# Optimization experiments

Hardware: AMD Instinct MI355X
Metric: run time of the kernel (lower is better)

Reference implementation:

```python
import jax, jax.numpy as jnp
import numpy as np

COMMITMENT_COST = 0.25


def setup_inputs() -> dict:
    key = jax.random.key(0)
    k1, k2 = jax.random.split(key)
    inputs = jax.random.normal(k1, (64, 4096, 64), dtype=jnp.float32)
    codewords = jax.random.normal(k2, (512, 64), dtype=jnp.float32)
    return {"inputs": inputs, "codewords": codewords}


def reference(inputs, codewords):
    D = codewords.shape[-1]
    flat = inputs.reshape(-1, D)  # (N, D)
    # squared Euclidean distances (N, K) via expansion, avoiding the (N, K, D) tensor
    x_sq = jnp.sum(flat * flat, axis=-1, keepdims=True)          # (N, 1)
    c_sq = jnp.sum(codewords * codewords, axis=-1)               # (K,)
    distances = x_sq - 2.0 * (flat @ codewords.T) + c_sq         # (N, K)
    encoding_indices = jnp.argmin(distances, axis=1)             # (N,)
    quantized = jnp.take(codewords, encoding_indices, axis=0).reshape(inputs.shape)
    commitment_loss = jnp.mean((jax.lax.stop_gradient(quantized) - inputs) ** 2)
    loss = COMMITMENT_COST * commitment_loss
    encoding_indices = encoding_indices.reshape(inputs.shape[:-1])
    return quantized, encoding_indices, loss
```

## Files before the change

kernel.cpp:

```cpp
#include <hip/hip_runtime.h>


typedef _Float16 half8 __attribute__((ext_vector_type(8)));
typedef float    floatx4 __attribute__((ext_vector_type(4)));

#define NVEC  262144
#define DDIM  64
#define KCW   512
#define LOSS_SCALE (0.25f / 16777216.0f)
#define DMARGIN 0.005f
#define BROWS 256
#define NBLK  (NVEC / BROWS)
#define CHUNK 256

#define SM_BS     0
#define SM_CSQH   69632
#define SM_WIN    71680
#define SM_LIST   72704
#define SM_FLG    73728
#define SM_RED    73984
#define SM_CNT    74016
#define SMEM_BYTES 74112

#define WS_CSQ   0
#define WS_CSQH  2048

__global__ void prep_kernel(const float* __restrict__ cw,
                            float* __restrict__ csq,
                            float* __restrict__ csqh,
                            float* __restrict__ loss_slot) {
    int n = blockIdx.x * blockDim.x + threadIdx.x;
    if (n < KCW) {
        const float4* r = (const float4*)(cw + n * DDIM);
        float s = 0.f;
        #pragma unroll
        for (int t = 0; t < 16; ++t) {
            float4 a = r[t];
            s += a.x * a.x + a.y * a.y + a.z * a.z + a.w * a.w;
        }
        csq[n]  = s;
        csqh[n] = 0.5f * s;
    }
    if (n == 0) *loss_slot = 0.f;
}

__global__ __launch_bounds__(512, 4)
void vq_mfma_kernel(const float* __restrict__ x,
                    const float* __restrict__ cw,
                    const float* __restrict__ csqh,
                    const float* __restrict__ csq,
                    float* __restrict__ out_q,
                    float* __restrict__ out_idx,
                    float* __restrict__ out_loss) {
    extern __shared__ char smem[];
    _Float16*      Bs     = (_Float16*)(smem + SM_BS);
    float*         csqhs  = (float*)(smem + SM_CSQH);
    int*           win    = (int*)(smem + SM_WIN);
    int*           lslist = (int*)(smem + SM_LIST);
    unsigned char* flg    = (unsigned char*)(smem + SM_FLG);
    float*         red    = (float*)(smem + SM_RED);
    unsigned*      lcnt   = (unsigned*)(smem + SM_CNT);

    const int tid  = threadIdx.x;
    const int w    = tid >> 6;
    const int lane = tid & 63;
    const int quad = lane >> 4;
    const int col  = lane & 15;
    const int blk  = blockIdx.x * BROWS;

    if (tid == 0) *lcnt = 0u;
    csqhs[tid] = -csqh[tid];

    half8 ah0[2], ah1[2], al0[2], al1[2];
    #pragma unroll
    for (int rt = 0; rt < 2; ++rt) {
        const float* xr = x + (size_t)(blk + w * 32 + rt * 16 + col) * DDIM;
        float4 f0 = *(const float4*)(xr + quad * 8);
        float4 f1 = *(const float4*)(xr + quad * 8 + 4);
        float4 g0 = *(const float4*)(xr + 32 + quad * 8);
        float4 g1 = *(const float4*)(xr + 32 + quad * 8 + 4);
        #pragma unroll
        for (int i = 0; i < 4; ++i) {
            float v = ((const float*)&f0)[i];
            _Float16 h = (_Float16)v;
            ah0[rt][i] = h; al0[rt][i] = (_Float16)(v - (float)h);
            v = ((const float*)&f1)[i]; h = (_Float16)v;
            ah0[rt][4 + i] = h; al0[rt][4 + i] = (_Float16)(v - (float)h);
            v = ((const float*)&g0)[i]; h = (_Float16)v;
            ah1[rt][i] = h; al1[rt][i] = (_Float16)(v - (float)h);
            v = ((const float*)&g1)[i]; h = (_Float16)v;
            ah1[rt][4 + i] = h; al1[rt][4 + i] = (_Float16)(v - (float)h);
        }
    }

    float M1[8], M2[8];
    int   idx[8];
    #pragma unroll
    for (int s = 0; s < 8; ++s) {
        M1[s] = -3.402823466e38f; M2[s] = -3.402823466e38f; idx[s] = 0;
    }

    for (int ch = 0; ch < 2; ++ch) {
        __syncthreads();
        {
            const int cidx = tid >> 1;
            const int hh   = tid & 1;
            const float4* src =
                (const float4*)(cw + (size_t)(ch * CHUNK + cidx) * DDIM + hh * 32);
            _Float16* dst = Bs + cidx * 136 + hh * 32;
            #pragma unroll
            for (int t = 0; t < 4; ++t) {
                float4 a = src[2 * t], b = src[2 * t + 1];
                half8 hv, lv;
                #pragma unroll
                for (int i = 0; i < 4; ++i) {
                    float v = ((const float*)&a)[i];
                    _Float16 h = (_Float16)v;
                    hv[i] = h; lv[i] = (_Float16)(v - (float)h);
                    v = ((const float*)&b)[i]; h = (_Float16)v;
                    hv[4 + i] = h; lv[4 + i] = (_Float16)(v - (float)h);
                }
                *(half8*)(dst + 8 * t) = hv;
                *(half8*)(dst + 64 + 8 * t) = lv;
            }
        }
        __syncthreads();

        #pragma unroll 2
        for (int t = 0; t < 16; ++t) {
            const int n  = ch * CHUNK + t * 16 + col;
            const int nb = (t * 16 + col) * 136;
            half8 bh0 = *(const half8*)&Bs[nb + quad * 8];
            half8 bh1 = *(const half8*)&Bs[nb + 32 + quad * 8];
            half8 bl0 = *(const half8*)&Bs[nb + 64 + quad * 8];
            half8 bl1 = *(const half8*)&Bs[nb + 96 + quad * 8];
            const float vn = csqhs[n];

            #pragma unroll
            for (int rt = 0; rt < 2; ++rt) {
                floatx4 acc = {vn, vn, vn, vn};
                acc = __builtin_amdgcn_mfma_f32_16x16x32_f16(ah0[rt], bh0, acc, 0, 0, 0);
                acc = __builtin_amdgcn_mfma_f32_16x16x32_f16(ah1[rt], bh1, acc, 0, 0, 0);
                acc = __builtin_amdgcn_mfma_f32_16x16x32_f16(al0[rt], bh0, acc, 0, 0, 0);
                acc = __builtin_amdgcn_mfma_f32_16x16x32_f16(al1[rt], bh1, acc, 0, 0, 0);
                acc = __builtin_amdgcn_mfma_f32_16x16x32_f16(ah0[rt], bl0, acc, 0, 0, 0);
                acc = __builtin_amdgcn_mfma_f32_16x16x32_f16(ah1[rt], bl1, acc, 0, 0, 0);
                #pragma unroll
                for (int reg = 0; reg < 4; ++reg) {
                    int s = rt * 4 + reg;
                    float d = acc[reg];
                    if (d > M1[s]) idx[s] = n;
                    M2[s] = __builtin_amdgcn_fmed3f(M1[s], M2[s], d);
                    M1[s] = fmaxf(M1[s], d);
                }
            }
        }
    }

    #pragma unroll
    for (int off = 1; off < 16; off <<= 1) {
        #pragma unroll
        for (int s = 0; s < 8; ++s) {
            float o1 = __shfl_xor(M1[s], off, 16);
            float o2 = __shfl_xor(M2[s], off, 16);
            int   oi = __shfl_xor(idx[s], off, 16);
            float mn = fminf(M1[s], o1);
            M2[s] = fmaxf(fmaxf(M2[s], o2), mn);
            if (o1 > M1[s] || (o1 == M1[s] && oi < idx[s])) idx[s] = oi;
            M1[s] = fmaxf(M1[s], o1);
        }
    }

    if (col < 4) {
        #pragma unroll
        for (int rt = 0; rt < 2; ++rt) {
            int s  = rt * 4 + col;
            int rl = w * 32 + rt * 16 + quad * 4 + col;
            int nw = idx[s];
            int f  = (M1[s] - M2[s] <= DMARGIN) ? 1 : 0;
            win[rl] = nw;
            flg[rl] = (unsigned char)f;
            out_idx[blk + rl] = (float)nw;
            if (f) { unsigned p = atomicAdd(lcnt, 1u); lslist[p] = rl; }
        }
    }
    __syncthreads();

    float ls = 0.f;
    #pragma unroll
    for (int k = 0; k < 8; ++k) {
        int rl = k * 32 + (tid >> 4);
        int e4 = (tid & 15) * 4;
        int wn = win[rl];
        int f  = flg[rl];
        float4 q  = *(const float4*)(cw + wn * DDIM + e4);
        float4 xv = *(const float4*)(x + (size_t)(blk + rl) * DDIM + e4);
        *(float4*)(out_q + (size_t)(blk + rl) * DDIM + e4) = q;
        if (!f) {
            float d0 = q.x - xv.x, d1 = q.y - xv.y;
            float d2 = q.z - xv.z, d3 = q.w - xv.w;
            ls += d0 * d0 + d1 * d1 + d2 * d2 + d3 * d3;
        }
    }
    #pragma unroll
    for (int off = 32; off > 0; off >>= 1) ls += __shfl_down(ls, off, 64);
    if (lane == 0) red[w] = ls;
    __syncthreads();
    if (tid == 0) {
        float s = 0.f;
        #pragma unroll
        for (int i = 0; i < 8; ++i) s += red[i];
        atomicAdd(out_loss, s * LOSS_SCALE);
    }

    const unsigned cnt = *lcnt;
    const int grp = tid >> 4;
    const int tx  = tid & 15;
    for (unsigned i = (unsigned)grp; i < cnt; i += 32) {
        const int rl = lslist[i];
        const size_t row = (size_t)blk + rl;

        float4 xr[16];
        const float4* xg = (const float4*)(x + row * DDIM);
        #pragma unroll
        for (int t = 0; t < 16; ++t) xr[t] = xg[t];

        float best = 3.402823466e38f; int bi = 0;
        for (int j = 0; j < 32; ++j) {
            int n = tx + 16 * j;
            const float4* c = (const float4*)(cw + n * DDIM);
            float a0 = 0.f, a1 = 0.f, a2 = 0.f, a3 = 0.f;
            #pragma unroll
            for (int t = 0; t < 16; ++t) {
                float4 cv = c[t];
                a0 = __builtin_fmaf(xr[t].x, cv.x, a0);
                a1 = __builtin_fmaf(xr[t].y, cv.y, a1);
                a2 = __builtin_fmaf(xr[t].z, cv.z, a2);
                a3 = __builtin_fmaf(xr[t].w, cv.w, a3);
            }
            float sc = __builtin_fmaf(-2.f, (a0 + a1) + (a2 + a3), csq[n]);
            if (sc < best) { best = sc; bi = n; }
        }
        #pragma unroll
        for (int off = 8; off > 0; off >>= 1) {
            float d2 = __shfl_down(best, off, 16);
            int   i2 = __shfl_down(bi,   off, 16);
            if (d2 < best || (d2 == best && i2 < bi)) { best = d2; bi = i2; }
        }
        if (tx == 0) {
            out_idx[row] = (float)bi;
            const float4* qg = (const float4*)(cw + bi * DDIM);
            float4* og = (float4*)(out_q + row * DDIM);
            float lf = 0.f;
            #pragma unroll
            for (int t = 0; t < 16; ++t) {
                float4 q = qg[t];
                og[t] = q;
                float d0 = q.x - xr[t].x, d1 = q.y - xr[t].y;
                float d2_ = q.z - xr[t].z, d3 = q.w - xr[t].w;
                lf += d0 * d0 + d1 * d1 + d2_ * d2_ + d3 * d3;
            }
            atomicAdd(out_loss, lf * LOSS_SCALE);
        }
    }
}

extern "C" void kernel_launch(void* const* d_in, const int* in_sizes, int n_in,
                              void* d_out, int out_size, void* d_ws, size_t ws_size,
                              hipStream_t stream) {
    const float* x  = (const float*)d_in[0];
    const float* cw = (const float*)d_in[1];
    float* out      = (float*)d_out;
    float* out_q    = out;
    float* out_idx  = out + 16777216;
    float* out_loss = out + 16777216 + 262144;

    char* ws = (char*)d_ws;
    float* csq  = (float*)(ws + WS_CSQ);
    float* csqh = (float*)(ws + WS_CSQH);

    (void)hipFuncSetAttribute((const void*)vq_mfma_kernel,
                              hipFuncAttributeMaxDynamicSharedMemorySize,
                              SMEM_BYTES);

    prep_kernel<<<8, 64, 0, stream>>>(cw, csq, csqh, out_loss);
    vq_mfma_kernel<<<NBLK, 512, SMEM_BYTES, stream>>>(x, cw, csqh, csq,
                                                      out_q, out_idx, out_loss);
}
```

Measured before the change: 239.7 us.

## Shrink codebook LDS chunk to 64 codewords with static shared memory

Staging now uses a 64-codeword chunk processed over 8 iterations instead of a 256-codeword chunk over 2, cutting the half-split codebook tile in LDS from about 68KB to about 17KB. Shared buffers become static, and the dynamic-LDS attribute call is dropped. The smaller LDS footprint is meant to let more 512-thread blocks share a CU and to drop the per-launch attribute call. The cost is four times as many block-wide barriers and load phases, with less MFMA work between each sync.

```diff
diff --git a/kernel.cpp b/kernel.cpp
--- a/kernel.cpp
+++ b/kernel.cpp
@@ -11,16 +11,7 @@
 #define DMARGIN 0.005f
 #define BROWS 256
 #define NBLK  (NVEC / BROWS)
-#define CHUNK 256
-
-#define SM_BS     0
-#define SM_CSQH   69632
-#define SM_WIN    71680
-#define SM_LIST   72704
-#define SM_FLG    73728
-#define SM_RED    73984
-#define SM_CNT    74016
-#define SMEM_BYTES 74112
+#define CHUNK 64
 
 #define WS_CSQ   0
 #define WS_CSQH  2048
@@ -52,14 +43,13 @@
                     float* __restrict__ out_q,
                     float* __restrict__ out_idx,
                     float* __restrict__ out_loss) {
-    extern __shared__ char smem[];
-    _Float16*      Bs     = (_Float16*)(smem + SM_BS);
-    float*         csqhs  = (float*)(smem + SM_CSQH);
-    int*           win    = (int*)(smem + SM_WIN);
-    int*           lslist = (int*)(smem + SM_LIST);
-    unsigned char* flg    = (unsigned char*)(smem + SM_FLG);
-    float*         red    = (float*)(smem + SM_RED);
-    unsigned*      lcnt   = (unsigned*)(smem + SM_CNT);
+    __shared__ _Float16      Bs[CHUNK * 136];
+    __shared__ float         csqhs[KCW];
+    __shared__ int           win[BROWS];
+    __shared__ int           lslist[BROWS];
+    __shared__ unsigned char flg[BROWS];
+    __shared__ float         red[8];
+    __shared__ unsigned      lcnt;
 
     const int tid  = threadIdx.x;
     const int w    = tid >> 6;
@@ -68,7 +58,7 @@
     const int col  = lane & 15;
     const int blk  = blockIdx.x * BROWS;
 
-    if (tid == 0) *lcnt = 0u;
+    if (tid == 0) lcnt = 0u;
     csqhs[tid] = -csqh[tid];
 
     half8 ah0[2], ah1[2], al0[2], al1[2];
@@ -100,34 +90,31 @@
         M1[s] = -3.402823466e38f; M2[s] = -3.402823466e38f; idx[s] = 0;
     }
 
-    for (int ch = 0; ch < 2; ++ch) {
+    for (int ch = 0; ch < 8; ++ch) {
         __syncthreads();
         {
-            const int cidx = tid >> 1;
-            const int hh   = tid & 1;
-            const float4* src =
-                (const float4*)(cw + (size_t)(ch * CHUNK + cidx) * DDIM + hh * 32);
-            _Float16* dst = Bs + cidx * 136 + hh * 32;
-            #pragma unroll
-            for (int t = 0; t < 4; ++t) {
-                float4 a = src[2 * t], b = src[2 * t + 1];
-                half8 hv, lv;
-                #pragma unroll
-                for (int i = 0; i < 4; ++i) {
-                    float v = ((const float*)&a)[i];
-                    _Float16 h = (_Float16)v;
-                    hv[i] = h; lv[i] = (_Float16)(v - (float)h);
-                    v = ((const float*)&b)[i]; h = (_Float16)v;
-                    hv[4 + i] = h; lv[4 + i] = (_Float16)(v - (float)h);
-                }
-                *(half8*)(dst + 8 * t) = hv;
-                *(half8*)(dst + 64 + 8 * t) = lv;
-            }
+            const int cidx = tid >> 3;
+            const int e8   = tid & 7;
+            const float* src =
+                cw + (size_t)(ch * CHUNK + cidx) * DDIM + e8 * 8;
+            float4 a = ((const float4*)src)[0];
+            float4 b = ((const float4*)src)[1];
+            half8 hv, lv;
+            #pragma unroll
+            for (int i = 0; i < 4; ++i) {
+                float v = ((const float*)&a)[i];
+                _Float16 h = (_Float16)v;
+                hv[i] = h; lv[i] = (_Float16)(v - (float)h);
+                v = ((const float*)&b)[i]; h = (_Float16)v;
+                hv[4 + i] = h; lv[4 + i] = (_Float16)(v - (float)h);
+            }
+            *(half8*)(Bs + cidx * 136 + e8 * 8)      = hv;
+            *(half8*)(Bs + cidx * 136 + 64 + e8 * 8) = lv;
         }
         __syncthreads();
 
         #pragma unroll 2
-        for (int t = 0; t < 16; ++t) {
+        for (int t = 0; t < 4; ++t) {
             const int n  = ch * CHUNK + t * 16 + col;
             const int nb = (t * 16 + col) * 136;
             half8 bh0 = *(const half8*)&Bs[nb + quad * 8];
@@ -181,7 +168,7 @@
             win[rl] = nw;
             flg[rl] = (unsigned char)f;
             out_idx[blk + rl] = (float)nw;
-            if (f) { unsigned p = atomicAdd(lcnt, 1u); lslist[p] = rl; }
+            if (f) { unsigned p = atomicAdd(&lcnt, 1u); lslist[p] = rl; }
         }
     }
     __syncthreads();
@@ -213,7 +200,7 @@
         atomicAdd(out_loss, s * LOSS_SCALE);
     }
 
-    const unsigned cnt = *lcnt;
+    const unsigned cnt = lcnt;
     const int grp = tid >> 4;
     const int tx  = tid & 15;
     for (unsigned i = (unsigned)grp; i < cnt; i += 32) {
@@ -279,11 +266,7 @@
     float* csq  = (float*)(ws + WS_CSQ);
     float* csqh = (float*)(ws + WS_CSQH);
 
-    (void)hipFuncSetAttribute((const void*)vq_mfma_kernel,
-                              hipFuncAttributeMaxDynamicSharedMemorySize,
-                              SMEM_BYTES);
-
-    prep_kernel<<<8, 64, 0, stream>>>(cw, csq, csqh, out_loss);
-    vq_mfma_kernel<<<NBLK, 512, SMEM_BYTES, stream>>>(x, cw, csqh, csq,
-                                                      out_q, out_idx, out_loss);
+    prep_kernel<<<2, 256, 0, stream>>>(cw, csq, csqh, out_loss);
+    vq_mfma_kernel<<<NBLK, 512, 0, stream>>>(x, cw, csqh, csq,
+                                             out_q, out_idx, out_loss);
 }
```

After: 228.8 us. -4.5%, faster.
